# Kernel tuning notes

Measured on AMD Instinct MI355X. Metric: run time of the kernel, lower is better.

Reference implementation:

```python
import jax, jax.numpy as jnp
import numpy as np

N, D, C = 4096, 512, 128
TOPK = 12  # rank-0 hard neg + up to 11 fallback ranks (torch loop breaks at loop_cnt>=10 -> max rank 11)


def setup_inputs() -> dict:
    key = jax.random.key(0)
    k1, k2, k3, k4, k5 = jax.random.split(key, 5)
    return {
        "inputs": jax.random.normal(k1, (N, D), jnp.float32),
        "prediction": jax.random.normal(k2, (N, C), jnp.float32),
        "targets": jax.random.randint(k3, (N,), 0, C),
        "true_targets": jax.random.randint(k4, (N,), 0, C),
        "prob": jax.random.uniform(k5, (N,), jnp.float32),
        "threshold": jnp.float32(0.5),
    }


def _gumbel_argmax(key, mask):
    # uniform random choice over True entries of each row (Gumbel-max trick)
    g = jax.random.gumbel(key, mask.shape, jnp.float32)
    return jnp.argmax(jnp.where(mask, g, -jnp.inf), axis=1)


def reference(inputs, prediction, targets, true_targets, prob, threshold):
    margin = jnp.float32(0.3)
    n = inputs.shape[0]
    rows = jnp.arange(n)
    # pairwise euclidean distance: ||xi||^2 + ||xj||^2 - 2 xi.xj, clamp+sqrt
    sq = jnp.sum(inputs * inputs, axis=1)
    d2 = sq[:, None] + sq[None, :] - 2.0 * (inputs @ inputs.T)
    dist = jnp.sqrt(jnp.clip(d2, 1e-12))  # [n, n]

    eye = jnp.eye(n, dtype=bool)
    same = targets[:, None] == targets[None, :]
    is_neg = ~same
    conf = prob >= threshold  # is_confident per anchor

    key = jax.random.key(42)
    kp, kp2 = jax.random.split(key)

    # random positive (!= i) and hardest negative per row
    ap_idx = _gumbel_argmax(kp, same & ~eye)
    neg_dist = jnp.where(is_neg, dist, jnp.inf)
    an_idx = jnp.argmin(neg_dist, axis=1)

    ap0 = dist[rows, ap_idx]
    an0 = dist[rows, an_idx]
    pos_conf = prob[ap_idx] >= threshold
    neg_conf = prob[an_idx] >= threshold
    # false-negative test: hard neg predicted as anchor's (noisy) label
    is_fn = jnp.argmax(prediction[an_idx], axis=1) == targets

    # case B (pos conf, neg unconf, FN): walk ranked negs for first confident one (ranks 1..11)
    nv, ni = jax.lax.top_k(-neg_dist, TOPK)  # smallest TOPK neg distances
    cand_conf = prob[ni] >= threshold
    tail = cand_conf[:, 1:]
    found = jnp.any(tail, axis=1)
    r = jnp.where(found, 1 + jnp.argmax(tail, axis=1), TOPK - 1)
    an_B = dist[rows, ni[rows, r]]

    # cases C / D-notFN: resample a confident positive (!= i); fallback to original pos
    conf_pos = same & ~eye & (prob >= threshold)[None, :]
    new_pos = jnp.where(jnp.any(conf_pos, axis=1), _gumbel_argmax(kp2, conf_pos), ap_idx)
    ap_new = dist[rows, new_pos]

    caseB = pos_conf & ~neg_conf & is_fn
    swap = (~pos_conf) & (neg_conf | ~is_fn)  # case C or case D-notFN
    inverse = (~pos_conf) & (~neg_conf) & is_fn

    half = (ap0 + an0) * 0.5
    ap = jnp.where(caseB, half, jnp.where(swap, ap_new, ap0))
    an = jnp.where(caseB, an_B, jnp.where(swap, half, an0))

    row_loss = jnp.where(inverse,
                         jax.nn.relu(an - ap + margin),
                         jax.nn.relu(ap - an + margin))
    cnt = jnp.sum(conf)
    loss = jnp.sum(jnp.where(conf, row_loss, 0.0)) / jnp.maximum(cnt, 1).astype(jnp.float32)
    correct = jnp.sum((an >= ap) & conf)
    return loss, correct
```

## Files before the change

### kernel.cpp

```cpp
#include <hip/hip_runtime.h>
#include <stdint.h>
#include <math.h>

#define N_ 4096
#define D_ 512
#define C_ 128
#define MAXC 256

typedef __attribute__((ext_vector_type(8))) short bf16x8;
typedef __attribute__((ext_vector_type(4))) float f32x4;

__host__ __device__ __forceinline__ uint32_t rotl32_(uint32_t x, int d) {
  return (x << d) | (x >> (32 - d));
}
__host__ __device__ inline void tf2x32(uint32_t k0, uint32_t k1,
                                       uint32_t x0, uint32_t x1,
                                       uint32_t& y0, uint32_t& y1) {
  const uint32_t k2 = k0 ^ k1 ^ 0x1BD11BDAu;
#define TF_R(rr) { x0 += x1; x1 = rotl32_(x1, rr); x1 ^= x0; }
  x0 += k0; x1 += k1;
  TF_R(13) TF_R(15) TF_R(26) TF_R(6)
  x0 += k1; x1 += k2 + 1u;
  TF_R(17) TF_R(29) TF_R(16) TF_R(24)
  x0 += k2; x1 += k0 + 2u;
  TF_R(13) TF_R(15) TF_R(26) TF_R(6)
  x0 += k0; x1 += k1 + 3u;
  TF_R(17) TF_R(29) TF_R(16) TF_R(24)
  x0 += k1; x1 += k2 + 4u;
  TF_R(13) TF_R(15) TF_R(26) TF_R(6)
  x0 += k2; x1 += k0 + 5u;
#undef TF_R
  y0 = x0; y1 = x1;
}

__device__ __forceinline__ float gumbel_ij(uint32_t k0, uint32_t k1, uint32_t m) {
  uint32_t y0, y1;
  tf2x32(k0, k1, 0u, m, y0, y1);
  uint32_t bits = y0 ^ y1;
  uint32_t vb = (bits >> 9) | 0x3f800000u;
  float f = __uint_as_float(vb) - 1.0f;
  float u = (f == 0.0f) ? 1.1754943508222875e-38f : f;
  return -logf(-logf(u));
}

__device__ __forceinline__ unsigned short f2bf(float x) {
  unsigned int b = __float_as_uint(x);
  b += 0x7fffu + ((b >> 16) & 1u);
  return (unsigned short)(b >> 16);
}
__device__ __forceinline__ float bf2f(unsigned short u) {
  return __uint_as_float(((unsigned int)u) << 16);
}

__device__ __forceinline__ void gll16(const void* g, void* lds) {
  __builtin_amdgcn_global_load_lds(
      (const __attribute__((address_space(1))) unsigned int*)g,
      (__attribute__((address_space(3))) unsigned int*)lds, 16, 0, 0);
}

__global__ void zero_k(float* __restrict__ accum, int* __restrict__ ccnt) {
  int t = threadIdx.x;
  if (t == 0) {
    accum[0] = 0.0f;
    ((unsigned*)accum)[1] = 0u;
    ((unsigned*)accum)[2] = 0u;
  }
  if (t < C_) ccnt[t] = 0;
}

__global__ __launch_bounds__(64) void prep_k(const float* __restrict__ inputs,
                                             const float* __restrict__ pred,
                                             const int* __restrict__ targets,
                                             float* __restrict__ sq,
                                             int* __restrict__ pam,
                                             int* __restrict__ ccnt,
                                             int* __restrict__ clist,
                                             unsigned short* __restrict__ XH,
                                             unsigned short* __restrict__ XL,
                                             int do_split, int do_list) {
  int i = blockIdx.x;
  int lane = threadIdx.x;
  const float4* rp = (const float4*)(inputs + (size_t)i * D_);
  float s = 0.0f;
#pragma unroll
  for (int q = 0; q < 2; ++q) {
    float4 v = rp[lane + 64 * q];
    s += v.x * v.x + v.y * v.y + v.z * v.z + v.w * v.w;
    if (do_split) {
      unsigned short h0 = f2bf(v.x), h1 = f2bf(v.y), h2 = f2bf(v.z), h3 = f2bf(v.w);
      unsigned short g0 = f2bf(v.x - bf2f(h0)), g1 = f2bf(v.y - bf2f(h1));
      unsigned short g2 = f2bf(v.z - bf2f(h2)), g3 = f2bf(v.w - bf2f(h3));
      uint2 hp, lp;
      hp.x = (unsigned)h0 | ((unsigned)h1 << 16); hp.y = (unsigned)h2 | ((unsigned)h3 << 16);
      lp.x = (unsigned)g0 | ((unsigned)g1 << 16); lp.y = (unsigned)g2 | ((unsigned)g3 << 16);
      size_t blk = ((size_t)(i >> 4) * 16 + ((lane >> 3) + 8 * q)) * 512;
      int lf = (i & 15) + 16 * ((lane & 7) >> 1);
      int j0 = 4 * (lane & 1);
      *(uint2*)&XH[blk + lf * 8 + j0] = hp;
      *(uint2*)&XL[blk + lf * 8 + j0] = lp;
    }
  }
#pragma unroll
  for (int off = 32; off; off >>= 1) s += __shfl_down(s, off);
  if (lane == 0) sq[i] = s;

  float v0 = pred[(size_t)i * C_ + lane];
  float v1 = pred[(size_t)i * C_ + 64 + lane];
  float bv; int bi;
  if (v1 > v0) { bv = v1; bi = lane + 64; } else { bv = v0; bi = lane; }
#pragma unroll
  for (int off = 32; off; off >>= 1) {
    float ov = __shfl_down(bv, off);
    int oi = __shfl_down(bi, off);
    if (ov > bv || (ov == bv && oi < bi)) { bv = ov; bi = oi; }
  }
  if (lane == 0) {
    pam[i] = bi;
    if (do_list) {
      int t = targets[i];
      int p = atomicAdd(&ccnt[t], 1);
      if (p < MAXC) clist[t * MAXC + p] = i;
    }
  }
}

__global__ __launch_bounds__(512, 3) void bigk5_k(const unsigned short* __restrict__ XH,
                                                  const unsigned short* __restrict__ XL,
                                                  const int* __restrict__ targets,
                                                  const float* __restrict__ sq,
                                                  float* __restrict__ pD,
                                                  int* __restrict__ pI) {
  __shared__ float U[18432];
  __shared__ float sqc[512];
  __shared__ int tcs[512];
  __shared__ float sqr[64];
  __shared__ int trs[64];

  short* AH = (short*)U;
  short* AL = AH + 2048;
  short* BH = AH + 4096;
  short* BL = BH + 16384;

  const int tid = threadIdx.x, w = tid >> 6, l = tid & 63;
  const int rb = blockIdx.x >> 3, sl = blockIdx.x & 7;
  const int rbase = rb * 64, cbase0 = sl * 512;

  sqc[tid] = sq[cbase0 + tid];
  tcs[tid] = targets[cbase0 + tid];
  if (tid < 64) { sqr[tid] = sq[rbase + tid]; trs[tid] = targets[rbase + tid]; }

  const int lo = l * 8;
  const size_t taw = (size_t)((rbase >> 4) + (w >> 1)) * 8192;
  const size_t tb0 = (size_t)((cbase0 >> 4) + w * 4) * 8192;

  f32x4 acc[4][4];
#pragma unroll
  for (int rt = 0; rt < 4; ++rt)
#pragma unroll
    for (int c = 0; c < 4; ++c) acc[rt][c] = (f32x4){0.f, 0.f, 0.f, 0.f};

  for (int kc = 0; kc < 16; ++kc) {
    const int off = kc * 512 + lo;
    __syncthreads();
    {
      const unsigned short* sp = (w & 1) ? XL : XH;
      short* dp = ((w & 1) ? AL : AH) + (w >> 1) * 512;
      gll16(sp + taw + off, dp);
    }
#pragma unroll
    for (int c = 0; c < 4; ++c) {
      size_t tb = tb0 + (size_t)c * 8192 + off;
      gll16(XH + tb, BH + (w * 4 + c) * 512);
      gll16(XL + tb, BL + (w * 4 + c) * 512);
    }
    __syncthreads();

    bf16x8 ah[4], am[4];
#pragma unroll
    for (int rt = 0; rt < 4; ++rt) {
      ah[rt] = *(const bf16x8*)(AH + rt * 512 + lo);
      am[rt] = *(const bf16x8*)(AL + rt * 512 + lo);
    }
#pragma unroll
    for (int c = 0; c < 4; ++c) {
      bf16x8 bh = *(const bf16x8*)(BH + (w * 4 + c) * 512 + lo);
      bf16x8 bl = *(const bf16x8*)(BL + (w * 4 + c) * 512 + lo);
#pragma unroll
      for (int rt = 0; rt < 4; ++rt) {
        acc[rt][c] = __builtin_amdgcn_mfma_f32_16x16x32_bf16(ah[rt], bh, acc[rt][c], 0, 0, 0);
        acc[rt][c] = __builtin_amdgcn_mfma_f32_16x16x32_bf16(ah[rt], bl, acc[rt][c], 0, 0, 0);
        acc[rt][c] = __builtin_amdgcn_mfma_f32_16x16x32_bf16(am[rt], bh, acc[rt][c], 0, 0, 0);
      }
    }
  }

  float* Dl = U;
  float dl[12]; int il[12];
#pragma unroll
  for (int q = 0; q < 12; ++q) { dl[q] = INFINITY; il[q] = 0; }
  const int srow = tid >> 3, u0 = tid & 7;
  const int orow = (l >> 4) * 4, lr = l & 15;

  for (int g = 0; g < 8; ++g) {
    __syncthreads();
    if (w == g) {
#pragma unroll
      for (int rt = 0; rt < 4; ++rt)
#pragma unroll
        for (int c = 0; c < 4; ++c)
#pragma unroll
          for (int r = 0; r < 4; ++r) {
            int row = rt * 16 + orow + r;
            int cl = c * 16 + lr;
            float d2 = sqr[row] + sqc[g * 64 + cl] - 2.0f * acc[rt][c][r];
            float d = (trs[row] == tcs[g * 64 + cl]) ? INFINITY : sqrtf(fmaxf(d2, 1e-12f));
            Dl[row * 68 + cl] = d;
          }
    }
    __syncthreads();
#pragma unroll
    for (int q = 0; q < 8; ++q) {
      int u = u0 + 8 * q;
      float d = Dl[srow * 68 + u];
      if (d < dl[11]) {
        int col = cbase0 + g * 64 + u;
        bool placed = false;
#pragma unroll
        for (int t = 11; t >= 1; --t) {
          if (!placed) {
            if (dl[t - 1] > d) { dl[t] = dl[t - 1]; il[t] = il[t - 1]; }
            else { dl[t] = d; il[t] = col; placed = true; }
          }
        }
        if (!placed) { dl[0] = d; il[0] = col; }
      }
    }
  }

  __syncthreads();
  float* MD = U;
  int* MI = (int*)(U + 6144);
#pragma unroll
  for (int q = 0; q < 12; ++q) { MD[tid * 12 + q] = dl[q]; MI[tid * 12 + q] = il[q]; }
  __syncthreads();
  if ((tid & 7) == 0) {
    int row = tid >> 3;
    int grow = rbase + row;
    float* outD = pD + ((size_t)grow * 8 + sl) * 12;
    int* outI = pI + ((size_t)grow * 8 + sl) * 12;
    int p0 = 0, p1 = 0, p2 = 0, p3 = 0, p4 = 0, p5 = 0, p6 = 0, p7 = 0;
    for (int o = 0; o < 12; ++o) {
      float bd = INFINITY; int bi = 0x7fffffff; int bs = 0;
#define HEADM(s, ps) if (ps < 12) { float d = MD[(row * 8 + (s)) * 12 + ps]; int ix = MI[(row * 8 + (s)) * 12 + ps]; if (d < bd || (d == bd && ix < bi)) { bd = d; bi = ix; bs = (s); } }
      HEADM(0, p0) HEADM(1, p1) HEADM(2, p2) HEADM(3, p3)
      HEADM(4, p4) HEADM(5, p5) HEADM(6, p6) HEADM(7, p7)
#undef HEADM
      outD[o] = bd; outI[o] = bi;
      if (bs == 0) p0++; else if (bs == 1) p1++; else if (bs == 2) p2++; else if (bs == 3) p3++;
      else if (bs == 4) p4++; else if (bs == 5) p5++; else if (bs == 6) p6++; else p7++;
    }
  }
}

__global__ __launch_bounds__(256, 2) void bigk_k(const float* __restrict__ inputs,
                                                 const int* __restrict__ targets,
                                                 const float* __restrict__ sq,
                                                 float* __restrict__ pD,
                                                 int* __restrict__ pI) {
  __shared__ float U[10496];
  __shared__ float sqc[256];
  __shared__ int tcs[256];
  __shared__ float sqr[64];
  __shared__ int trs[64];

  float* Al = U;
  float* Bl = U + 2176;
  float* Dl = U;
  float* MD = U;
  int* MI = (int*)(U + 3072);

  const int tid = threadIdx.x;
  const int rb = blockIdx.x >> 3, sl = blockIdx.x & 7;
  const int rbase = rb * 64, cbase0 = sl * 512;

  if (tid < 64) { sqr[tid] = sq[rbase + tid]; trs[tid] = targets[rbase + tid]; }

  float dl[12]; int il[12];
#pragma unroll
  for (int q = 0; q < 12; ++q) { dl[q] = INFINITY; il[q] = 0; }

  const int w = tid >> 6, lane = tid & 63;
  const int rg = lane >> 3, cg = lane & 7;
  const int r0 = rg * 8, c0l = w * 64 + cg * 8;
  const int srow = tid >> 2, scq = tid & 3;

  for (int ci = 0; ci < 2; ++ci) {
    const int cbase = cbase0 + ci * 256;
    __syncthreads();
    sqc[tid] = sq[cbase + tid];
    tcs[tid] = targets[cbase + tid];

    float acc[8][8];
#pragma unroll
    for (int a = 0; a < 8; ++a)
#pragma unroll
      for (int b = 0; b < 8; ++b) acc[a][b] = 0.0f;

    for (int kc = 0; kc < 16; ++kc) {
      const int kb = kc * 32;
      __syncthreads();
#pragma unroll
      for (int q = 0; q < 2; ++q) {
        int idx = tid + 256 * q;
        int row = idx >> 3, kq = idx & 7;
        float4 v = *(const float4*)(inputs + (size_t)(rbase + row) * D_ + kb + kq * 4);
        Al[(4 * kq + 0) * 68 + row] = v.x;
        Al[(4 * kq + 1) * 68 + row] = v.y;
        Al[(4 * kq + 2) * 68 + row] = v.z;
        Al[(4 * kq + 3) * 68 + row] = v.w;
      }
#pragma unroll
      for (int q = 0; q < 8; ++q) {
        int idx = tid + 256 * q;
        int col = idx >> 3, kq = idx & 7;
        float4 v = *(const float4*)(inputs + (size_t)(cbase + col) * D_ + kb + kq * 4);
        Bl[(4 * kq + 0) * 260 + col] = v.x;
        Bl[(4 * kq + 1) * 260 + col] = v.y;
        Bl[(4 * kq + 2) * 260 + col] = v.z;
        Bl[(4 * kq + 3) * 260 + col] = v.w;
      }
      __syncthreads();
#pragma unroll 4
      for (int k = 0; k < 32; ++k) {
        float4 a0 = *(const float4*)&Al[k * 68 + r0];
        float4 a1 = *(const float4*)&Al[k * 68 + r0 + 4];
        float4 b0 = *(const float4*)&Bl[k * 260 + c0l];
        float4 b1 = *(const float4*)&Bl[k * 260 + c0l + 4];
        float a_[8] = {a0.x, a0.y, a0.z, a0.w, a1.x, a1.y, a1.z, a1.w};
        float b_[8] = {b0.x, b0.y, b0.z, b0.w, b1.x, b1.y, b1.z, b1.w};
#pragma unroll
        for (int ii = 0; ii < 8; ++ii)
#pragma unroll
          for (int jj = 0; jj < 8; ++jj)
            acc[ii][jj] = fmaf(a_[ii], b_[jj], acc[ii][jj]);
      }
    }

    for (int h = 0; h < 2; ++h) {
      __syncthreads();
#pragma unroll
      for (int i = 0; i < 8; ++i) {
        float si = sqr[r0 + i];
        int ti_ = trs[r0 + i];
#pragma unroll
        for (int jj = 0; jj < 4; ++jj) {
          int j = 4 * h + jj;
          float d2 = si + sqc[c0l + j] - 2.0f * acc[i][j];
          float d = (ti_ == tcs[c0l + j]) ? INFINITY : sqrtf(fmaxf(d2, 1e-12f));
          Dl[(r0 + i) * 129 + (w * 32 + cg * 4 + jj)] = d;
        }
      }
      __syncthreads();
      for (int q = 0; q < 32; ++q) {
        float d = Dl[srow * 129 + scq * 32 + q];
        if (d < dl[11]) {
          int u = scq * 32 + q;
          int col = cbase + ((u >> 5) << 6) + (((u >> 2) & 7) << 3) + (h << 2) + (u & 3);
          bool placed = false;
#pragma unroll
          for (int t = 11; t >= 1; --t) {
            if (!placed) {
              if (dl[t - 1] > d) { dl[t] = dl[t - 1]; il[t] = il[t - 1]; }
              else { dl[t] = d; il[t] = col; placed = true; }
            }
          }
          if (!placed) { dl[0] = d; il[0] = col; }
        }
      }
    }
  }

  __syncthreads();
#pragma unroll
  for (int q = 0; q < 12; ++q) { MD[tid * 12 + q] = dl[q]; MI[tid * 12 + q] = il[q]; }
  __syncthreads();
  if ((tid & 3) == 0) {
    int row = tid >> 2;
    int grow = rbase + row;
    float* outD = pD + ((size_t)grow * 8 + sl) * 12;
    int* outI = pI + ((size_t)grow * 8 + sl) * 12;
    int p0 = 0, p1 = 0, p2 = 0, p3 = 0;
    for (int o = 0; o < 12; ++o) {
      float bd = INFINITY; int bi = 0x7fffffff; int bc = 0;
      if (p0 < 12) { float d = MD[(row * 4 + 0) * 12 + p0]; int ix = MI[(row * 4 + 0) * 12 + p0]; if (d < bd || (d == bd && ix < bi)) { bd = d; bi = ix; bc = 0; } }
      if (p1 < 12) { float d = MD[(row * 4 + 1) * 12 + p1]; int ix = MI[(row * 4 + 1) * 12 + p1]; if (d < bd || (d == bd && ix < bi)) { bd = d; bi = ix; bc = 1; } }
      if (p2 < 12) { float d = MD[(row * 4 + 2) * 12 + p2]; int ix = MI[(row * 4 + 2) * 12 + p2]; if (d < bd || (d == bd && ix < bi)) { bd = d; bi = ix; bc = 2; } }
      if (p3 < 12) { float d = MD[(row * 4 + 3) * 12 + p3]; int ix = MI[(row * 4 + 3) * 12 + p3]; if (d < bd || (d == bd && ix < bi)) { bd = d; bi = ix; bc = 3; } }
      outD[o] = bd; outI[o] = bi;
      if (bc == 0) p0++; else if (bc == 1) p1++; else if (bc == 2) p2++; else p3++;
    }
  }
}

__device__ __forceinline__ float wdist2(float4 xi0, float4 xi1,
                                        const float* __restrict__ inputs,
                                        const float* __restrict__ sq,
                                        int i, int j, int lane) {
  const float4* b = (const float4*)(inputs + (size_t)j * D_);
  float4 y0 = b[lane], y1 = b[lane + 64];
  float s = xi0.x * y0.x + xi0.y * y0.y + xi0.z * y0.z + xi0.w * y0.w +
            xi1.x * y1.x + xi1.y * y1.y + xi1.z * y1.z + xi1.w * y1.w;
#pragma unroll
  for (int off = 32; off; off >>= 1) s += __shfl_xor(s, off);
  float d2 = sq[i] + sq[j] - 2.0f * s;
  return sqrtf(fmaxf(d2, 1e-12f));
}

__global__ __launch_bounds__(256) void finalize_k(const float* __restrict__ inputs,
                                                  const int* __restrict__ targets,
                                                  const float* __restrict__ prob,
                                                  const float* __restrict__ thr_p,
                                                  const float* __restrict__ sq,
                                                  const int* __restrict__ pam,
                                                  const float* __restrict__ pD,
                                                  const int* __restrict__ pI,
                                                  const int* __restrict__ ccnt,
                                                  const int* __restrict__ clist,
                                                  float* __restrict__ accum,
                                                  uint32_t kp0, uint32_t kp1,
                                                  uint32_t kq0, uint32_t kq1,
                                                  int use_list) {
  const int wid = threadIdx.x >> 6, lane = threadIdx.x & 63;
  const int i = blockIdx.x * 4 + wid;
  const float thr = *thr_p;
  const int ti = targets[i];

  float g1 = -INFINITY; int i1 = 0;
  float g2 = -INFINITY; int i2 = 0;
  int f2 = 0;
  if (use_list) {
    int cnt = ccnt[ti]; if (cnt > MAXC) cnt = MAXC;
    const int* lst = clist + (size_t)ti * MAXC;
    for (int base = 0; base < cnt; base += 64) {
      int idx = base + lane;
      if (idx < cnt) {
        int j = lst[idx];
        if (j != i) {
          uint32_t m = ((uint32_t)i << 12) | (uint32_t)j;
          float g = gumbel_ij(kp0, kp1, m);
          if (g > g1 || (g == g1 && j < i1)) { g1 = g; i1 = j; }
          if (prob[j] >= thr) {
            float gg = gumbel_ij(kq0, kq1, m);
            if (gg > g2 || (gg == g2 && j < i2)) { g2 = gg; i2 = j; }
            f2 = 1;
          }
        }
      }
    }
  } else {
    for (int j = lane; j < N_; j += 64) {
      if (targets[j] == ti && j != i) {
        uint32_t m = ((uint32_t)i << 12) | (uint32_t)j;
        float g = gumbel_ij(kp0, kp1, m);
        if (g > g1 || (g == g1 && j < i1)) { g1 = g; i1 = j; }
        if (prob[j] >= thr) {
          float gg = gumbel_ij(kq0, kq1, m);
          if (gg > g2 || (gg == g2 && j < i2)) { g2 = gg; i2 = j; }
          f2 = 1;
        }
      }
    }
  }
#pragma unroll
  for (int off = 32; off; off >>= 1) {
    float og = __shfl_xor(g1, off); int oi = __shfl_xor(i1, off);
    if (og > g1 || (og == g1 && oi < i1)) { g1 = og; i1 = oi; }
    float oh = __shfl_xor(g2, off); int oj = __shfl_xor(i2, off);
    if (oh > g2 || (oh == g2 && oj < i2)) { g2 = oh; i2 = oj; }
  }
  f2 = __any(f2);
  const int ap_idx = i1;
  const int new_pos = f2 ? i2 : ap_idx;

  const float4* arow = (const float4*)(inputs + (size_t)i * D_);
  float4 xi0 = arow[lane], xi1 = arow[lane + 64];
  const float ap0 = wdist2(xi0, xi1, inputs, sq, i, ap_idx, lane);
  const float ap_new = wdist2(xi0, xi1, inputs, sq, i, new_pos, lane);

  const float* rowD = pD + (size_t)i * 96;
  const int* rowI = pI + (size_t)i * 96;
  int ci_[12];
  {
    int p0 = 0, p1 = 0, p2 = 0, p3 = 0, p4 = 0, p5 = 0, p6 = 0, p7 = 0;
#pragma unroll
    for (int o = 0; o < 12; ++o) {
      float bd = INFINITY; int bi = 0x7fffffff; int bs = 0;
#define HEADQ(s, ps) if (ps < 12) { float d = rowD[(s) * 12 + ps]; int ix = rowI[(s) * 12 + ps]; if (d < bd || (d == bd && ix < bi)) { bd = d; bi = ix; bs = (s); } }
      HEADQ(0, p0) HEADQ(1, p1) HEADQ(2, p2) HEADQ(3, p3)
      HEADQ(4, p4) HEADQ(5, p5) HEADQ(6, p6) HEADQ(7, p7)
#undef HEADQ
      ci_[o] = bi;
      if (bs == 0) p0++; else if (bs == 1) p1++; else if (bs == 2) p2++; else if (bs == 3) p3++;
      else if (bs == 4) p4++; else if (bs == 5) p5++; else if (bs == 6) p6++; else p7++;
    }
  }
  float de[12];
#pragma unroll
  for (int o = 0; o < 12; ++o) de[o] = wdist2(xi0, xi1, inputs, sq, i, ci_[o], lane);

  float an0 = de[0]; int an_idx = ci_[0]; int minpos = 0;
#pragma unroll
  for (int o = 1; o < 12; ++o)
    if (de[o] < an0 || (de[o] == an0 && ci_[o] < an_idx)) { an0 = de[o]; an_idx = ci_[o]; minpos = o; }
  float anB = INFINITY; int anBi = 0x7fffffff; bool fB = false;
#pragma unroll
  for (int o = 0; o < 12; ++o) {
    if (o != minpos) {
      bool cf = prob[ci_[o]] >= thr;
      if (cf && (de[o] < anB || (de[o] == anB && ci_[o] < anBi))) { anB = de[o]; anBi = ci_[o]; fB = true; }
    }
  }
  if (!fB) {
    anB = de[0]; anBi = ci_[0];
#pragma unroll
    for (int o = 1; o < 12; ++o)
      if (de[o] > anB || (de[o] == anB && ci_[o] > anBi)) { anB = de[o]; anBi = ci_[o]; }
  }
  const float an_B = anB;

  if (lane == 0) {
    bool neg_conf = prob[an_idx] >= thr;
    bool pos_conf = prob[ap_idx] >= thr;
    bool is_fn = (pam[an_idx] == ti);
    bool caseB = pos_conf && !neg_conf && is_fn;
    bool swap_ = !pos_conf && (neg_conf || !is_fn);
    bool inverse = !pos_conf && !neg_conf && is_fn;
    float half = 0.5f * (ap0 + an0);
    float ap = caseB ? half : (swap_ ? ap_new : ap0);
    float an = caseB ? an_B : (swap_ ? half : an0);
    const float margin = 0.3f;
    float rl = inverse ? fmaxf(an - ap + margin, 0.0f) : fmaxf(ap - an + margin, 0.0f);
    bool conf_i = prob[i] >= thr;
    if (conf_i) {
      atomicAdd(&accum[0], rl);
      atomicAdd(((unsigned*)accum) + 2, 1u);
      if (an >= ap) atomicAdd(((unsigned*)accum) + 1, 1u);
    }
  }
}

__global__ void writeout_k(const float* __restrict__ accum, float* __restrict__ out) {
  unsigned correct = ((const unsigned*)accum)[1];
  unsigned cnt = ((const unsigned*)accum)[2];
  out[0] = accum[0] / fmaxf((float)cnt, 1.0f);
  out[1] = (float)correct;
}

extern "C" void kernel_launch(void* const* d_in, const int* in_sizes, int n_in,
                              void* d_out, int out_size, void* d_ws, size_t ws_size,
                              hipStream_t stream) {
  const float* inputs = (const float*)d_in[0];
  const float* pred = (const float*)d_in[1];
  const int* targets = (const int*)d_in[2];
  const float* prob = (const float*)d_in[4];
  const float* thr = (const float*)d_in[5];
  float* out = (float*)d_out;

  float* sq = (float*)d_ws;
  int* pam = (int*)d_ws + N_;
  float* pD = (float*)d_ws + 2 * N_;
  int* pI = (int*)d_ws + 2 * N_ + N_ * 96;
  float* accum = (float*)d_ws + 2 * N_ + 2 * (N_ * 96);
  int* ccnt = (int*)accum + 16;
  int* clist = ccnt + C_;
  const size_t base_f = (size_t)(2 * N_ + 2 * (N_ * 96) + 16 + C_ + C_ * MAXC);
  const size_t split_off = ((base_f * 4 + 15) / 16) * 16;
  unsigned short* XH = (unsigned short*)((char*)d_ws + split_off);
  unsigned short* XL = XH + (size_t)N_ * D_;
  const size_t need = split_off + (size_t)2 * N_ * D_ * 2;
  const int use_v2 = (ws_size >= need) ? 1 : 0;

  uint32_t kp0, kp1, kq0, kq1;
  tf2x32(0u, 42u, 0u, 0u, kp0, kp1);
  tf2x32(0u, 42u, 0u, 1u, kq0, kq1);

  zero_k<<<dim3(1), dim3(128), 0, stream>>>(accum, ccnt);
  prep_k<<<dim3(N_), dim3(64), 0, stream>>>(inputs, pred, targets, sq, pam, ccnt, clist,
                                            XH, XL, use_v2, use_v2);
  if (use_v2)
    bigk5_k<<<dim3(512), dim3(512), 0, stream>>>(XH, XL, targets, sq, pD, pI);
  else
    bigk_k<<<dim3(512), dim3(256), 0, stream>>>(inputs, targets, sq, pD, pI);
  finalize_k<<<dim3(N_ / 4), dim3(256), 0, stream>>>(inputs, targets, prob, thr, sq, pam,
                                                     pD, pI, ccnt, clist, accum,
                                                     kp0, kp1, kq0, kq1, use_v2);
  writeout_k<<<dim3(1), dim3(1), 0, stream>>>(accum, out);
}
```

Measured before the change: 394.2 us.

## Double-buffer LDS tiles in pairwise-distance GEMM to overlap loads with MFMA

Replaces the single-buffered shared-memory staging in the bf16-split distance GEMM with two buffers. The loads for the next K-chunk are issued before the MFMAs on the current chunk, and one barrier per iteration replaces two. The goal is to hide global-to-LDS load latency behind matrix work. The cost is that the shared array doubles to roughly 147 KB and the launch bound drops the min-blocks hint, so only one 512-thread block likely fits per CU instead of three. That occupancy loss may cancel the overlap.

```diff
diff --git a/kernel.cpp b/kernel.cpp
--- a/kernel.cpp
+++ b/kernel.cpp
@@ -124,23 +124,18 @@
   }
 }
 
-__global__ __launch_bounds__(512, 3) void bigk5_k(const unsigned short* __restrict__ XH,
-                                                  const unsigned short* __restrict__ XL,
-                                                  const int* __restrict__ targets,
-                                                  const float* __restrict__ sq,
-                                                  float* __restrict__ pD,
-                                                  int* __restrict__ pI) {
-  __shared__ float U[18432];
+__global__ __launch_bounds__(512) void bigk6_k(const unsigned short* __restrict__ XH,
+                                               const unsigned short* __restrict__ XL,
+                                               const int* __restrict__ targets,
+                                               const float* __restrict__ sq,
+                                               float* __restrict__ pD,
+                                               int* __restrict__ pI) {
+  __shared__ float U[36864];
   __shared__ float sqc[512];
   __shared__ int tcs[512];
   __shared__ float sqr[64];
   __shared__ int trs[64];
 
-  short* AH = (short*)U;
-  short* AL = AH + 2048;
-  short* BH = AH + 4096;
-  short* BL = BH + 16384;
-
   const int tid = threadIdx.x, w = tid >> 6, l = tid & 63;
   const int rb = blockIdx.x >> 3, sl = blockIdx.x & 7;
   const int rbase = rb * 64, cbase0 = sl * 512;
@@ -152,39 +147,47 @@
   const int lo = l * 8;
   const size_t taw = (size_t)((rbase >> 4) + (w >> 1)) * 8192;
   const size_t tb0 = (size_t)((cbase0 >> 4) + w * 4) * 8192;
-
-  f32x4 acc[4][4];
-#pragma unroll
-  for (int rt = 0; rt < 4; ++rt)
-#pragma unroll
-    for (int c = 0; c < 4; ++c) acc[rt][c] = (f32x4){0.f, 0.f, 0.f, 0.f};
-
-  for (int kc = 0; kc < 16; ++kc) {
+  const unsigned short* aplane = (w & 1) ? XL : XH;
+  short* bufs = (short*)U;
+  const int adst = (w & 1) * 2048 + (w >> 1) * 512;
+
+  auto stage = [&](int b, int kc) {
+    short* base = bufs + b * 36864;
     const int off = kc * 512 + lo;
-    __syncthreads();
-    {
-      const unsigned short* sp = (w & 1) ? XL : XH;
-      short* dp = ((w & 1) ? AL : AH) + (w >> 1) * 512;
-      gll16(sp + taw + off, dp);
-    }
+    gll16(aplane + taw + off, base + adst);
 #pragma unroll
     for (int c = 0; c < 4; ++c) {
       size_t tb = tb0 + (size_t)c * 8192 + off;
-      gll16(XH + tb, BH + (w * 4 + c) * 512);
-      gll16(XL + tb, BL + (w * 4 + c) * 512);
-    }
-    __syncthreads();
-
+      gll16(XH + tb, base + 4096 + (w * 4 + c) * 512);
+      gll16(XL + tb, base + 20480 + (w * 4 + c) * 512);
+    }
+  };
+
+  f32x4 acc[4][4];
+#pragma unroll
+  for (int rt = 0; rt < 4; ++rt)
+#pragma unroll
+    for (int c = 0; c < 4; ++c) acc[rt][c] = (f32x4){0.f, 0.f, 0.f, 0.f};
+
+  stage(0, 0);
+  __syncthreads();
+  int cur = 0;
+  for (int kc = 0; kc < 16; ++kc) {
+    if (kc < 15) stage(cur ^ 1, kc + 1);
+    short* AHc = bufs + cur * 36864;
+    short* ALc = AHc + 2048;
+    short* BHc = AHc + 4096;
+    short* BLc = AHc + 20480;
     bf16x8 ah[4], am[4];
 #pragma unroll
     for (int rt = 0; rt < 4; ++rt) {
-      ah[rt] = *(const bf16x8*)(AH + rt * 512 + lo);
-      am[rt] = *(const bf16x8*)(AL + rt * 512 + lo);
+      ah[rt] = *(const bf16x8*)(AHc + rt * 512 + lo);
+      am[rt] = *(const bf16x8*)(ALc + rt * 512 + lo);
     }
 #pragma unroll
     for (int c = 0; c < 4; ++c) {
-      bf16x8 bh = *(const bf16x8*)(BH + (w * 4 + c) * 512 + lo);
-      bf16x8 bl = *(const bf16x8*)(BL + (w * 4 + c) * 512 + lo);
+      bf16x8 bh = *(const bf16x8*)(BHc + (w * 4 + c) * 512 + lo);
+      bf16x8 bl = *(const bf16x8*)(BLc + (w * 4 + c) * 512 + lo);
 #pragma unroll
       for (int rt = 0; rt < 4; ++rt) {
         acc[rt][c] = __builtin_amdgcn_mfma_f32_16x16x32_bf16(ah[rt], bh, acc[rt][c], 0, 0, 0);
@@ -192,6 +195,8 @@
         acc[rt][c] = __builtin_amdgcn_mfma_f32_16x16x32_bf16(am[rt], bh, acc[rt][c], 0, 0, 0);
       }
     }
+    __syncthreads();
+    cur ^= 1;
   }
 
   float* Dl = U;
@@ -588,7 +593,7 @@
   prep_k<<<dim3(N_), dim3(64), 0, stream>>>(inputs, pred, targets, sq, pam, ccnt, clist,
                                             XH, XL, use_v2, use_v2);
   if (use_v2)
-    bigk5_k<<<dim3(512), dim3(512), 0, stream>>>(XH, XL, targets, sq, pD, pI);
+    bigk6_k<<<dim3(512), dim3(512), 0, stream>>>(XH, XL, targets, sq, pD, pI);
   else
     bigk_k<<<dim3(512), dim3(256), 0, stream>>>(inputs, targets, sq, pD, pI);
   finalize_k<<<dim3(N_ / 4), dim3(256), 0, stream>>>(inputs, targets, prob, thr, sq, pam,
```

After: 441.7 us. 1.12x slower.
